# Performance work log

Hardware: AMD Instinct MI355X
Metric: run time of the kernel (lower is better)

The kernel has to match this reference:

```python
import jax, jax.numpy as jnp
import numpy as np

IN_CH, OUT_CH, KH, KW = 512, 512, 3, 3
LR_MULT = 1.0
WEIGHT_SCALE = LR_MULT / np.sqrt(IN_CH * KH * KW)


def setup_inputs() -> dict:
    key = jax.random.key(0)
    k1, k2, k3 = jax.random.split(key, 3)
    x = jax.random.normal(k1, (16, IN_CH, 32, 32), dtype=jnp.float32)
    s = jax.random.normal(k2, (16, IN_CH), dtype=jnp.float32)
    weight = jax.random.normal(k3, (OUT_CH, IN_CH, KH, KW), dtype=jnp.float32) / LR_MULT
    return {"x": x, "s": s, "weight": weight}


def reference(x, s, weight):
    B, Cin, H, Wd = x.shape
    Cout = weight.shape[0]
    W = weight * WEIGHT_SCALE                          # [Cout, Cin, kH, kW]
    # per-sample modulation: [B, Cout, Cin, kH, kW]
    Wm = s[:, None, :, None, None] * W[None]
    # demodulation: normalize each (b, out_channel) filter
    sigma = jnp.sqrt(jnp.sum(Wm ** 2, axis=(-3, -2, -1), keepdims=True) + 1e-8)
    Wm = Wm / sigma
    # grouped conv with groups = B
    x_g = x.reshape(1, B * Cin, H, Wd)
    W_g = Wm.reshape(B * Cout, Cin, KH, KW)
    out = jax.lax.conv_general_dilated(
        x_g, W_g,
        window_strides=(1, 1),
        padding="SAME",
        rhs_dilation=(1, 1),
        feature_group_count=B,
        dimension_numbers=("NCHW", "OIHW", "NCHW"),
    )
    return out.reshape(B, Cout, out.shape[-2], out.shape[-1])
```

## Files before the change

kernel.cpp:

```cpp
#include <hip/hip_runtime.h>
#include <hip/hip_bf16.h>


typedef __attribute__((ext_vector_type(4))) float f32x4;
typedef __attribute__((ext_vector_type(8))) short bf16x8;

#define NB    16
#define CIN   512
#define COUT  512
#define KTOT  4608
#define NPIX  (NB * 32 * 32)

__device__ __forceinline__ void gload_lds16(const void* g, void* l) {
  __builtin_amdgcn_global_load_lds(
      (__attribute__((address_space(1))) void*)(g),
      (__attribute__((address_space(3))) void*)(l), 16, 0, 0);
}

__global__ __launch_bounds__(256) void pack_w_kernel(
    const float* __restrict__ w, __hip_bfloat16* __restrict__ wB,
    float* __restrict__ wsq) {
  const int idx = blockIdx.x * 256 + threadIdx.x;
  const int o = idx >> 9, ci = idx & 511;
  const float* wp = w + (size_t)idx * 9;
  const float WSCALE = 0.014731391274719739f;
  float sum = 0.f;
#pragma unroll
  for (int t = 0; t < 9; ++t) {
    float v = wp[t] * WSCALE;
    sum += v * v;
    wB[(size_t)o * KTOT + t * 512 + ci] = __float2bfloat16(v);
  }
  wsq[idx] = sum;
}

__global__ __launch_bounds__(256) void calc_rsig_kernel(
    const float* __restrict__ s, const float* __restrict__ wsq,
    float* __restrict__ rsig) {
  const int wid = blockIdx.x * 4 + (threadIdx.x >> 6);
  const int lane = threadIdx.x & 63;
  const int b = wid >> 9, o = wid & 511;
  const float* sp = s + b * 512;
  const float* wp = wsq + o * 512;
  float sum = 0.f;
#pragma unroll
  for (int i = 0; i < 8; ++i) {
    float sv = sp[lane + i * 64];
    sum += sv * sv * wp[lane + i * 64];
  }
#pragma unroll
  for (int off = 32; off > 0; off >>= 1) sum += __shfl_down(sum, off, 64);
  if (lane == 0) rsig[wid] = 1.0f / sqrtf(sum + 1e-8f);
}

__global__ __launch_bounds__(256) void modulate_kernel(
    const float* __restrict__ x, const float* __restrict__ s,
    __hip_bfloat16* __restrict__ xpad) {
  const int by = blockIdx.x;
  const int b = by >> 5, y = by & 31;
  __shared__ __attribute__((aligned(16))) __hip_bfloat16 tile[32][72];
  const int tid = threadIdx.x;
  const int xc = tid & 31;
  const int cr0 = tid >> 5;
  const float* xrow = x + ((size_t)b * 512 * 32 + y) * 32;
  const float* sb = s + b * 512;
  __hip_bfloat16* orow = xpad + (size_t)((b * 34 + y + 1) * 34) * 512;

  for (int ci0 = 0; ci0 < 512; ci0 += 64) {
#pragma unroll
    for (int r = 0; r < 8; ++r) {
      const int cir = r * 8 + cr0;
      const int ci = ci0 + cir;
      float v = xrow[(size_t)ci * 1024 + xc] * sb[ci];
      tile[xc][cir] = __float2bfloat16(v);
    }
    __syncthreads();
    const int xcw = tid >> 3, vec = tid & 7;
    bf16x8 v = *(const bf16x8*)&tile[xcw][vec * 8];
    *(bf16x8*)(orow + (size_t)(xcw + 1) * 512 + ci0 + vec * 8) = v;
    __syncthreads();
  }
}

__global__ __launch_bounds__(256, 2) void conv_gemm_kernel(
    const __hip_bfloat16* __restrict__ wB,
    const __hip_bfloat16* __restrict__ xpad,
    const float* __restrict__ rsig,
    float* __restrict__ out,
    __hip_bfloat16* __restrict__ p1) {
  __shared__ __attribute__((aligned(16))) __hip_bfloat16 ldsA[128 * 64];
  __shared__ __attribute__((aligned(16))) __hip_bfloat16 ldsB[256 * 64];

  const int tid = threadIdx.x;
  const int wv = tid >> 6, lane = tid & 63, l15 = lane & 15;
  const int bo0 = blockIdx.y << 7;
  const int bp0 = blockIdx.x << 8;
  const int z = blockIdx.z;
  const int bimg = blockIdx.x >> 2;
  const int wr = wv >> 1, wc = wv & 1;

  int gA[4];
#pragma unroll
  for (int r = 0; r < 4; ++r) {
    const int c = r * 256 + tid, row = c >> 3, sc = (c & 7) ^ (row & 7);
    gA[r] = (bo0 + row) * KTOT + sc * 8;
  }
  int gB[8];
#pragma unroll
  for (int r = 0; r < 8; ++r) {
    const int c = r * 256 + tid, row = c >> 3, sc = (c & 7) ^ (row & 7);
    const int p = bp0 + row, b = p >> 10, rem = p & 1023, y = rem >> 5,
              xx = rem & 31;
    gB[r] = ((b * 34 + y) * 34 + xx) * 512 + sc * 8;
  }

  f32x4 acc[4][8];
#pragma unroll
  for (int mi = 0; mi < 4; ++mi)
#pragma unroll
    for (int ni = 0; ni < 8; ++ni) acc[mi][ni] = f32x4{0.f, 0.f, 0.f, 0.f};

  const int kb0 = (lane >> 4) << 4;

#pragma unroll 1
  for (int kt = 0; kt < 36; ++kt) {
    const int ktg = z * 36 + kt;
    const int tap = ktg >> 3;
    const int xoff = (tap + 31 * (tap / 3)) * 512 + ((ktg & 7) << 6);
#pragma unroll
    for (int r = 0; r < 4; ++r)
      gload_lds16(wB + (size_t)(gA[r] + (ktg << 6)),
                  (char*)ldsA + (r * 256 + tid) * 16);
#pragma unroll
    for (int r = 0; r < 8; ++r)
      gload_lds16(xpad + (size_t)(gB[r] + xoff),
                  (char*)ldsB + (r * 256 + tid) * 16);
    __syncthreads();

    bf16x8 af[4][2];
#pragma unroll
    for (int mi = 0; mi < 4; ++mi) {
      const int row = (wr << 6) + (mi << 4) + l15;
      const int swz = (row & 7) << 4;
      af[mi][0] = *(const bf16x8*)((const char*)ldsA + row * 128 + (kb0 ^ swz));
      af[mi][1] = *(const bf16x8*)((const char*)ldsA + row * 128 + ((64 | kb0) ^ swz));
    }
    {
      bf16x8 bv[8];
#pragma unroll
      for (int ni = 0; ni < 8; ++ni) {
        const int row = (wc << 7) + (ni << 4) + l15;
        bv[ni] = *(const bf16x8*)((const char*)ldsB + row * 128 +
                                  (kb0 ^ ((row & 7) << 4)));
      }
#pragma unroll
      for (int mi = 0; mi < 4; ++mi)
#pragma unroll
        for (int ni = 0; ni < 8; ++ni)
          acc[mi][ni] = __builtin_amdgcn_mfma_f32_16x16x32_bf16(
              af[mi][0], bv[ni], acc[mi][ni], 0, 0, 0);
    }
    {
      bf16x8 bv[8];
#pragma unroll
      for (int ni = 0; ni < 8; ++ni) {
        const int row = (wc << 7) + (ni << 4) + l15;
        bv[ni] = *(const bf16x8*)((const char*)ldsB + row * 128 +
                                  ((64 | kb0) ^ ((row & 7) << 4)));
      }
#pragma unroll
      for (int mi = 0; mi < 4; ++mi)
#pragma unroll
        for (int ni = 0; ni < 8; ++ni)
          acc[mi][ni] = __builtin_amdgcn_mfma_f32_16x16x32_bf16(
              af[mi][1], bv[ni], acc[mi][ni], 0, 0, 0);
    }
    __syncthreads();
  }

#pragma unroll
  for (int mi = 0; mi < 4; ++mi) {
    const int o = bo0 + (wr << 6) + (mi << 4) + ((lane >> 4) << 2);
    const f32x4 rs = *(const f32x4*)(rsig + (bimg << 9) + o);
#pragma unroll
    for (int ni = 0; ni < 8; ++ni) {
      const int p = bp0 + (wc << 7) + (ni << 4) + l15;
      const int prem = p & 1023;
      if (z == 0) {
#pragma unroll
        for (int r = 0; r < 4; ++r)
          out[((size_t)(bimg << 9) + o + r) * 1024 + prem] =
              acc[mi][ni][r] * rs[r];
      } else {
#pragma unroll
        for (int r = 0; r < 4; ++r)
          p1[((size_t)(bimg << 9) + o + r) * 1024 + prem] =
              __float2bfloat16(acc[mi][ni][r] * rs[r]);
      }
    }
  }
}

__global__ __launch_bounds__(256) void merge_kernel(
    float* __restrict__ out, const __hip_bfloat16* __restrict__ p1) {
  const int i = blockIdx.x * 256 + threadIdx.x;
  f32x4* o4 = (f32x4*)out + 2 * (size_t)i;
  f32x4 a = o4[0], b = o4[1];
  const bf16x8 pv = ((const bf16x8*)p1)[i];
#pragma unroll
  for (int j = 0; j < 4; ++j) {
    a[j] += __uint_as_float(((unsigned)(unsigned short)pv[j]) << 16);
    b[j] += __uint_as_float(((unsigned)(unsigned short)pv[4 + j]) << 16);
  }
  o4[0] = a;
  o4[1] = b;
}

extern "C" void kernel_launch(void* const* d_in, const int* in_sizes, int n_in,
                              void* d_out, int out_size, void* d_ws,
                              size_t ws_size, hipStream_t stream) {
  const float* x = (const float*)d_in[0];
  const float* s = (const float*)d_in[1];
  const float* w = (const float*)d_in[2];
  float* out = (float*)d_out;

  char* ws = (char*)d_ws;
  const size_t xpad_bytes = (size_t)NB * 34 * 34 * 512 * 2;
  const size_t wB_bytes = (size_t)COUT * KTOT * 2;
  const size_t wsq_bytes = (size_t)COUT * CIN * 4;
  const size_t rsig_bytes = (size_t)NB * COUT * 4;
  __hip_bfloat16* xpad = (__hip_bfloat16*)ws;
  __hip_bfloat16* wB = (__hip_bfloat16*)(ws + xpad_bytes);
  float* wsq = (float*)(ws + xpad_bytes + wB_bytes);
  float* rsig = (float*)(ws + xpad_bytes + wB_bytes + wsq_bytes);
  __hip_bfloat16* p1 =
      (__hip_bfloat16*)(ws + xpad_bytes + wB_bytes + wsq_bytes + rsig_bytes);

  hipMemsetAsync(xpad, 0, xpad_bytes, stream);
  pack_w_kernel<<<(COUT * CIN) / 256, 256, 0, stream>>>(w, wB, wsq);
  modulate_kernel<<<NB * 32, 256, 0, stream>>>(x, s, xpad);
  calc_rsig_kernel<<<(NB * COUT) / 4, 256, 0, stream>>>(s, wsq, rsig);
  conv_gemm_kernel<<<dim3(NPIX / 256, COUT / 128, 2), 256, 0, stream>>>(
      wB, xpad, rsig, out, p1);
  merge_kernel<<<(NPIX * COUT / 8) / 256, 256, 0, stream>>>(out, p1);
}
```

Baseline: 105.6 us.

## Drop split-K and merge kernel; add triple-buffered LDS prefetch pipeline

Measured after the change: 112.3 us. +6.3%, slower.

```diff
diff --git a/kernel.cpp b/kernel.cpp
--- a/kernel.cpp
+++ b/kernel.cpp
@@ -10,6 +10,13 @@
 #define COUT  512
 #define KTOT  4608
 #define NPIX  (NB * 32 * 32)
+#define KTILES 72
+#define BUFBYTES 49152
+
+#define WAITV12() asm volatile("s_waitcnt vmcnt(12)" ::: "memory")
+#define WAITV0()  asm volatile("s_waitcnt vmcnt(0)" ::: "memory")
+#define FENCE()   asm volatile("" ::: "memory")
+#define BAR()     { FENCE(); __builtin_amdgcn_s_barrier(); FENCE(); }
 
 __device__ __forceinline__ void gload_lds16(const void* g, void* l) {
   __builtin_amdgcn_global_load_lds(
@@ -82,20 +89,17 @@
   }
 }
 
-__global__ __launch_bounds__(256, 2) void conv_gemm_kernel(
+__global__ __launch_bounds__(256, 1) void conv_gemm_kernel(
     const __hip_bfloat16* __restrict__ wB,
     const __hip_bfloat16* __restrict__ xpad,
     const float* __restrict__ rsig,
-    float* __restrict__ out,
-    __hip_bfloat16* __restrict__ p1) {
-  __shared__ __attribute__((aligned(16))) __hip_bfloat16 ldsA[128 * 64];
-  __shared__ __attribute__((aligned(16))) __hip_bfloat16 ldsB[256 * 64];
+    float* __restrict__ out) {
+  extern __shared__ __attribute__((aligned(16))) char ldsc[];
 
   const int tid = threadIdx.x;
   const int wv = tid >> 6, lane = tid & 63, l15 = lane & 15;
   const int bo0 = blockIdx.y << 7;
   const int bp0 = blockIdx.x << 8;
-  const int z = blockIdx.z;
   const int bimg = blockIdx.x >> 2;
   const int wr = wv >> 1, wc = wv & 1;
 
@@ -114,44 +118,54 @@
     gB[r] = ((b * 34 + y) * 34 + xx) * 512 + sc * 8;
   }
 
-  f32x4 acc[4][8];
-#pragma unroll
-  for (int mi = 0; mi < 4; ++mi)
-#pragma unroll
-    for (int ni = 0; ni < 8; ++ni) acc[mi][ni] = f32x4{0.f, 0.f, 0.f, 0.f};
-
-  const int kb0 = (lane >> 4) << 4;
-
-#pragma unroll 1
-  for (int kt = 0; kt < 36; ++kt) {
-    const int ktg = z * 36 + kt;
-    const int tap = ktg >> 3;
-    const int xoff = (tap + 31 * (tap / 3)) * 512 + ((ktg & 7) << 6);
+  auto stage = [&](int kt) {
+    char* base = ldsc + (kt % 3) * BUFBYTES;
+    const int tap = kt >> 3;
+    const int xoff = (tap + 31 * (tap / 3)) * 512 + ((kt & 7) << 6);
 #pragma unroll
     for (int r = 0; r < 4; ++r)
-      gload_lds16(wB + (size_t)(gA[r] + (ktg << 6)),
-                  (char*)ldsA + (r * 256 + tid) * 16);
+      gload_lds16(wB + (size_t)(gA[r] + (kt << 6)),
+                  base + (r * 256 + tid) * 16);
 #pragma unroll
     for (int r = 0; r < 8; ++r)
       gload_lds16(xpad + (size_t)(gB[r] + xoff),
-                  (char*)ldsB + (r * 256 + tid) * 16);
-    __syncthreads();
+                  base + 16384 + (r * 256 + tid) * 16);
+  };
+
+  f32x4 acc[4][8];
+#pragma unroll
+  for (int mi = 0; mi < 4; ++mi)
+#pragma unroll
+    for (int ni = 0; ni < 8; ++ni) acc[mi][ni] = f32x4{0.f, 0.f, 0.f, 0.f};
+
+  const int kb0 = (lane >> 4) << 4;
+
+  stage(0);
+  stage(1);
+
+#pragma unroll 1
+  for (int kt = 0; kt < KTILES; ++kt) {
+    if (kt < KTILES - 1) { WAITV12(); } else { WAITV0(); }
+    BAR();
+    if (kt + 2 < KTILES) stage(kt + 2);
+
+    const char* bufA = ldsc + (kt % 3) * BUFBYTES;
+    const char* bufB = bufA + 16384;
 
     bf16x8 af[4][2];
 #pragma unroll
     for (int mi = 0; mi < 4; ++mi) {
       const int row = (wr << 6) + (mi << 4) + l15;
       const int swz = (row & 7) << 4;
-      af[mi][0] = *(const bf16x8*)((const char*)ldsA + row * 128 + (kb0 ^ swz));
-      af[mi][1] = *(const bf16x8*)((const char*)ldsA + row * 128 + ((64 | kb0) ^ swz));
+      af[mi][0] = *(const bf16x8*)(bufA + row * 128 + (kb0 ^ swz));
+      af[mi][1] = *(const bf16x8*)(bufA + row * 128 + ((64 | kb0) ^ swz));
     }
     {
       bf16x8 bv[8];
 #pragma unroll
       for (int ni = 0; ni < 8; ++ni) {
         const int row = (wc << 7) + (ni << 4) + l15;
-        bv[ni] = *(const bf16x8*)((const char*)ldsB + row * 128 +
-                                  (kb0 ^ ((row & 7) << 4)));
+        bv[ni] = *(const bf16x8*)(bufB + row * 128 + (kb0 ^ ((row & 7) << 4)));
       }
 #pragma unroll
       for (int mi = 0; mi < 4; ++mi)
@@ -165,7 +179,7 @@
 #pragma unroll
       for (int ni = 0; ni < 8; ++ni) {
         const int row = (wc << 7) + (ni << 4) + l15;
-        bv[ni] = *(const bf16x8*)((const char*)ldsB + row * 128 +
+        bv[ni] = *(const bf16x8*)(bufB + row * 128 +
                                   ((64 | kb0) ^ ((row & 7) << 4)));
       }
 #pragma unroll
@@ -175,7 +189,6 @@
           acc[mi][ni] = __builtin_amdgcn_mfma_f32_16x16x32_bf16(
               af[mi][1], bv[ni], acc[mi][ni], 0, 0, 0);
     }
-    __syncthreads();
   }
 
 #pragma unroll
@@ -186,34 +199,12 @@
     for (int ni = 0; ni < 8; ++ni) {
       const int p = bp0 + (wc << 7) + (ni << 4) + l15;
       const int prem = p & 1023;
-      if (z == 0) {
-#pragma unroll
-        for (int r = 0; r < 4; ++r)
-          out[((size_t)(bimg << 9) + o + r) * 1024 + prem] =
-              acc[mi][ni][r] * rs[r];
-      } else {
-#pragma unroll
-        for (int r = 0; r < 4; ++r)
-          p1[((size_t)(bimg << 9) + o + r) * 1024 + prem] =
-              __float2bfloat16(acc[mi][ni][r] * rs[r]);
-      }
-    }
-  }
-}
-
-__global__ __launch_bounds__(256) void merge_kernel(
-    float* __restrict__ out, const __hip_bfloat16* __restrict__ p1) {
-  const int i = blockIdx.x * 256 + threadIdx.x;
-  f32x4* o4 = (f32x4*)out + 2 * (size_t)i;
-  f32x4 a = o4[0], b = o4[1];
-  const bf16x8 pv = ((const bf16x8*)p1)[i];
-#pragma unroll
-  for (int j = 0; j < 4; ++j) {
-    a[j] += __uint_as_float(((unsigned)(unsigned short)pv[j]) << 16);
-    b[j] += __uint_as_float(((unsigned)(unsigned short)pv[4 + j]) << 16);
-  }
-  o4[0] = a;
-  o4[1] = b;
+#pragma unroll
+      for (int r = 0; r < 4; ++r)
+        out[((size_t)(bimg << 9) + o + r) * 1024 + prem] =
+            acc[mi][ni][r] * rs[r];
+    }
+  }
 }
 
 extern "C" void kernel_launch(void* const* d_in, const int* in_sizes, int n_in,
@@ -228,19 +219,19 @@
   const size_t xpad_bytes = (size_t)NB * 34 * 34 * 512 * 2;
   const size_t wB_bytes = (size_t)COUT * KTOT * 2;
   const size_t wsq_bytes = (size_t)COUT * CIN * 4;
-  const size_t rsig_bytes = (size_t)NB * COUT * 4;
   __hip_bfloat16* xpad = (__hip_bfloat16*)ws;
   __hip_bfloat16* wB = (__hip_bfloat16*)(ws + xpad_bytes);
   float* wsq = (float*)(ws + xpad_bytes + wB_bytes);
   float* rsig = (float*)(ws + xpad_bytes + wB_bytes + wsq_bytes);
-  __hip_bfloat16* p1 =
-      (__hip_bfloat16*)(ws + xpad_bytes + wB_bytes + wsq_bytes + rsig_bytes);
+
+  const int lds_bytes = 3 * BUFBYTES;
+  hipFuncSetAttribute((const void*)conv_gemm_kernel,
+                      hipFuncAttributeMaxDynamicSharedMemorySize, lds_bytes);
 
   hipMemsetAsync(xpad, 0, xpad_bytes, stream);
   pack_w_kernel<<<(COUT * CIN) / 256, 256, 0, stream>>>(w, wB, wsq);
   modulate_kernel<<<NB * 32, 256, 0, stream>>>(x, s, xpad);
   calc_rsig_kernel<<<(NB * COUT) / 4, 256, 0, stream>>>(s, wsq, rsig);
-  conv_gemm_kernel<<<dim3(NPIX / 256, COUT / 128, 2), 256, 0, stream>>>(
-      wB, xpad, rsig, out, p1);
-  merge_kernel<<<(NPIX * COUT / 8) / 256, 256, 0, stream>>>(out, p1);
-}
+  conv_gemm_kernel<<<dim3(NPIX / 256, COUT / 128), 256, lds_bytes, stream>>>(
+      wB, xpad, rsig, out);
+}
```

## Switch conv GEMM to 32x32x16 MFMA with fragment-ordered LDS, halo-only zeroing, bf16 partials

Applied to the files above, without the earlier changes.

Result: slower. 142.3 us (+34.8%).

```diff
diff --git a/kernel.cpp b/kernel.cpp
--- a/kernel.cpp
+++ b/kernel.cpp
@@ -3,6 +3,7 @@
 
 
 typedef __attribute__((ext_vector_type(4))) float f32x4;
+typedef __attribute__((ext_vector_type(16))) float f32x16;
 typedef __attribute__((ext_vector_type(8))) short bf16x8;
 
 #define NB    16
@@ -15,6 +16,10 @@
   __builtin_amdgcn_global_load_lds(
       (__attribute__((address_space(1))) void*)(g),
       (__attribute__((address_space(3))) void*)(l), 16, 0, 0);
+}
+
+__device__ __forceinline__ float bf16bits_to_f32(short v) {
+  return __uint_as_float(((unsigned)(unsigned short)v) << 16);
 }
 
 __global__ __launch_bounds__(256) void pack_w_kernel(
@@ -82,17 +87,31 @@
   }
 }
 
+__global__ __launch_bounds__(256) void halo_zero_kernel(
+    __hip_bfloat16* __restrict__ xpad) {
+  const int sb = blockIdx.x;
+  const int b = sb / 132, s = sb - b * 132;
+  int y, x;
+  if (s < 34)       { y = 0;        x = s; }
+  else if (s < 68)  { y = 33;       x = s - 34; }
+  else if (s < 100) { y = s - 67;   x = 0; }
+  else              { y = s - 99;   x = 33; }
+  unsigned* p = (unsigned*)(xpad + (size_t)((b * 34 + y) * 34 + x) * 512);
+  p[threadIdx.x] = 0u;
+}
+
 __global__ __launch_bounds__(256, 2) void conv_gemm_kernel(
     const __hip_bfloat16* __restrict__ wB,
     const __hip_bfloat16* __restrict__ xpad,
     const float* __restrict__ rsig,
     float* __restrict__ out,
+    __hip_bfloat16* __restrict__ p0,
     __hip_bfloat16* __restrict__ p1) {
-  __shared__ __attribute__((aligned(16))) __hip_bfloat16 ldsA[128 * 64];
-  __shared__ __attribute__((aligned(16))) __hip_bfloat16 ldsB[256 * 64];
+  __shared__ __attribute__((aligned(16))) char ldsc[49152];
 
   const int tid = threadIdx.x;
-  const int wv = tid >> 6, lane = tid & 63, l15 = lane & 15;
+  const int wv = tid >> 6, lane = tid & 63;
+  const int l31 = lane & 31, lhi = lane >> 5;
   const int bo0 = blockIdx.y << 7;
   const int bp0 = blockIdx.x << 8;
   const int z = blockIdx.z;
@@ -102,25 +121,29 @@
   int gA[4];
 #pragma unroll
   for (int r = 0; r < 4; ++r) {
-    const int c = r * 256 + tid, row = c >> 3, sc = (c & 7) ^ (row & 7);
-    gA[r] = (bo0 + row) * KTOT + sc * 8;
+    const int u = r * 256 + tid, frag = u >> 6, l = u & 63;
+    const int fi = frag >> 2, ks = frag & 3;
+    const int row = fi * 32 + (l & 31), k = ks * 16 + (l >> 5) * 8;
+    gA[r] = (bo0 + row) * KTOT + k;
   }
   int gB[8];
 #pragma unroll
   for (int r = 0; r < 8; ++r) {
-    const int c = r * 256 + tid, row = c >> 3, sc = (c & 7) ^ (row & 7);
-    const int p = bp0 + row, b = p >> 10, rem = p & 1023, y = rem >> 5,
+    const int u = r * 256 + tid, frag = u >> 6, l = u & 63;
+    const int ni = frag >> 2, ks = frag & 3;
+    const int pr = ni * 32 + (l & 31), k = ks * 16 + (l >> 5) * 8;
+    const int p = bp0 + pr, b = p >> 10, rem = p & 1023, y = rem >> 5,
               xx = rem & 31;
-    gB[r] = ((b * 34 + y) * 34 + xx) * 512 + sc * 8;
-  }
-
-  f32x4 acc[4][8];
-#pragma unroll
-  for (int mi = 0; mi < 4; ++mi)
-#pragma unroll
-    for (int ni = 0; ni < 8; ++ni) acc[mi][ni] = f32x4{0.f, 0.f, 0.f, 0.f};
-
-  const int kb0 = (lane >> 4) << 4;
+    gB[r] = ((b * 34 + y) * 34 + xx) * 512 + k;
+  }
+
+  f32x16 acc[2][4];
+#pragma unroll
+  for (int mi = 0; mi < 2; ++mi)
+#pragma unroll
+    for (int ni = 0; ni < 4; ++ni)
+#pragma unroll
+      for (int e = 0; e < 16; ++e) acc[mi][ni][e] = 0.f;
 
 #pragma unroll 1
   for (int kt = 0; kt < 36; ++kt) {
@@ -130,87 +153,89 @@
 #pragma unroll
     for (int r = 0; r < 4; ++r)
       gload_lds16(wB + (size_t)(gA[r] + (ktg << 6)),
-                  (char*)ldsA + (r * 256 + tid) * 16);
+                  ldsc + (r * 256 + tid) * 16);
 #pragma unroll
     for (int r = 0; r < 8; ++r)
       gload_lds16(xpad + (size_t)(gB[r] + xoff),
-                  (char*)ldsB + (r * 256 + tid) * 16);
-    __syncthreads();
-
-    bf16x8 af[4][2];
-#pragma unroll
-    for (int mi = 0; mi < 4; ++mi) {
-      const int row = (wr << 6) + (mi << 4) + l15;
-      const int swz = (row & 7) << 4;
-      af[mi][0] = *(const bf16x8*)((const char*)ldsA + row * 128 + (kb0 ^ swz));
-      af[mi][1] = *(const bf16x8*)((const char*)ldsA + row * 128 + ((64 | kb0) ^ swz));
+                  ldsc + 16384 + (r * 256 + tid) * 16);
+    __syncthreads();
+
+    bf16x8 av[2][4];
+#pragma unroll
+    for (int mi = 0; mi < 2; ++mi)
+#pragma unroll
+      for (int ks = 0; ks < 4; ++ks)
+        av[mi][ks] = *(const bf16x8*)(
+            ldsc + (((wr * 2 + mi) * 4 + ks) << 10) + lane * 16);
+#pragma unroll
+    for (int ks = 0; ks < 4; ++ks) {
+      bf16x8 bv[4];
+#pragma unroll
+      for (int ni = 0; ni < 4; ++ni)
+        bv[ni] = *(const bf16x8*)(
+            ldsc + 16384 + (((wc * 4 + ni) * 4 + ks) << 10) + lane * 16);
+#pragma unroll
+      for (int mi = 0; mi < 2; ++mi)
+#pragma unroll
+        for (int ni = 0; ni < 4; ++ni)
+          acc[mi][ni] = __builtin_amdgcn_mfma_f32_32x32x16_bf16(
+              av[mi][ks], bv[ni], acc[mi][ni], 0, 0, 0);
     }
-    {
-      bf16x8 bv[8];
-#pragma unroll
-      for (int ni = 0; ni < 8; ++ni) {
-        const int row = (wc << 7) + (ni << 4) + l15;
-        bv[ni] = *(const bf16x8*)((const char*)ldsB + row * 128 +
-                                  (kb0 ^ ((row & 7) << 4)));
-      }
-#pragma unroll
-      for (int mi = 0; mi < 4; ++mi)
-#pragma unroll
-        for (int ni = 0; ni < 8; ++ni)
-          acc[mi][ni] = __builtin_amdgcn_mfma_f32_16x16x32_bf16(
-              af[mi][0], bv[ni], acc[mi][ni], 0, 0, 0);
-    }
-    {
-      bf16x8 bv[8];
-#pragma unroll
-      for (int ni = 0; ni < 8; ++ni) {
-        const int row = (wc << 7) + (ni << 4) + l15;
-        bv[ni] = *(const bf16x8*)((const char*)ldsB + row * 128 +
-                                  ((64 | kb0) ^ ((row & 7) << 4)));
-      }
-#pragma unroll
-      for (int mi = 0; mi < 4; ++mi)
-#pragma unroll
-        for (int ni = 0; ni < 8; ++ni)
-          acc[mi][ni] = __builtin_amdgcn_mfma_f32_16x16x32_bf16(
-              af[mi][1], bv[ni], acc[mi][ni], 0, 0, 0);
-    }
-    __syncthreads();
-  }
-
-#pragma unroll
-  for (int mi = 0; mi < 4; ++mi) {
-    const int o = bo0 + (wr << 6) + (mi << 4) + ((lane >> 4) << 2);
-    const f32x4 rs = *(const f32x4*)(rsig + (bimg << 9) + o);
-#pragma unroll
-    for (int ni = 0; ni < 8; ++ni) {
-      const int p = bp0 + (wc << 7) + (ni << 4) + l15;
-      const int prem = p & 1023;
-      if (z == 0) {
-#pragma unroll
-        for (int r = 0; r < 4; ++r)
-          out[((size_t)(bimg << 9) + o + r) * 1024 + prem] =
-              acc[mi][ni][r] * rs[r];
-      } else {
-#pragma unroll
-        for (int r = 0; r < 4; ++r)
-          p1[((size_t)(bimg << 9) + o + r) * 1024 + prem] =
-              __float2bfloat16(acc[mi][ni][r] * rs[r]);
+    __syncthreads();
+  }
+
+  __hip_bfloat16* pz = z ? p1 : p0;
+  const bool f32path = (p0 == nullptr) && (z == 0);
+#pragma unroll
+  for (int mi = 0; mi < 2; ++mi) {
+    const int obase = bo0 + (wr << 6) + (mi << 5);
+#pragma unroll
+    for (int q = 0; q < 4; ++q) {
+      const int r4 = q * 8 + lhi * 4;
+      const f32x4 rs = *(const f32x4*)(rsig + (bimg << 9) + obase + r4);
+#pragma unroll
+      for (int ni = 0; ni < 4; ++ni) {
+        const int p = bp0 + (wc << 7) + (ni << 5) + l31;
+        const int prem = p & 1023;
+#pragma unroll
+        for (int j = 0; j < 4; ++j) {
+          const float v = acc[mi][ni][q * 4 + j] * rs[j];
+          const size_t oidx =
+              ((size_t)((bimg << 9) + obase + r4 + j)) * 1024 + prem;
+          if (f32path) out[oidx] = v;
+          else pz[oidx] = __float2bfloat16(v);
+        }
       }
     }
   }
 }
 
-__global__ __launch_bounds__(256) void merge_kernel(
+__global__ __launch_bounds__(256) void merge2_kernel(
+    float* __restrict__ out, const __hip_bfloat16* __restrict__ p0,
+    const __hip_bfloat16* __restrict__ p1) {
+  const size_t i = (size_t)blockIdx.x * 256 + threadIdx.x;
+  const bf16x8 a = ((const bf16x8*)p0)[i];
+  const bf16x8 b = ((const bf16x8*)p1)[i];
+  f32x4 o0, o1;
+#pragma unroll
+  for (int j = 0; j < 4; ++j) {
+    o0[j] = bf16bits_to_f32(a[j]) + bf16bits_to_f32(b[j]);
+    o1[j] = bf16bits_to_f32(a[4 + j]) + bf16bits_to_f32(b[4 + j]);
+  }
+  ((f32x4*)out)[2 * i] = o0;
+  ((f32x4*)out)[2 * i + 1] = o1;
+}
+
+__global__ __launch_bounds__(256) void merge1_kernel(
     float* __restrict__ out, const __hip_bfloat16* __restrict__ p1) {
-  const int i = blockIdx.x * 256 + threadIdx.x;
-  f32x4* o4 = (f32x4*)out + 2 * (size_t)i;
+  const size_t i = (size_t)blockIdx.x * 256 + threadIdx.x;
+  f32x4* o4 = (f32x4*)out + 2 * i;
   f32x4 a = o4[0], b = o4[1];
   const bf16x8 pv = ((const bf16x8*)p1)[i];
 #pragma unroll
   for (int j = 0; j < 4; ++j) {
-    a[j] += __uint_as_float(((unsigned)(unsigned short)pv[j]) << 16);
-    b[j] += __uint_as_float(((unsigned)(unsigned short)pv[4 + j]) << 16);
+    a[j] += bf16bits_to_f32(pv[j]);
+    b[j] += bf16bits_to_f32(pv[4 + j]);
   }
   o4[0] = a;
   o4[1] = b;
@@ -229,18 +254,27 @@
   const size_t wB_bytes = (size_t)COUT * KTOT * 2;
   const size_t wsq_bytes = (size_t)COUT * CIN * 4;
   const size_t rsig_bytes = (size_t)NB * COUT * 4;
+  const size_t part_bytes = (size_t)NPIX * COUT * 2;
   __hip_bfloat16* xpad = (__hip_bfloat16*)ws;
   __hip_bfloat16* wB = (__hip_bfloat16*)(ws + xpad_bytes);
   float* wsq = (float*)(ws + xpad_bytes + wB_bytes);
   float* rsig = (float*)(ws + xpad_bytes + wB_bytes + wsq_bytes);
-  __hip_bfloat16* p1 =
-      (__hip_bfloat16*)(ws + xpad_bytes + wB_bytes + wsq_bytes + rsig_bytes);
-
-  hipMemsetAsync(xpad, 0, xpad_bytes, stream);
+  char* pbase = ws + xpad_bytes + wB_bytes + wsq_bytes + rsig_bytes;
+  __hip_bfloat16* p1 = (__hip_bfloat16*)pbase;
+  __hip_bfloat16* p0 = (__hip_bfloat16*)(pbase + part_bytes);
+  const bool two_partials =
+      ws_size >= (xpad_bytes + wB_bytes + wsq_bytes + rsig_bytes +
+                  2 * part_bytes);
+
+  halo_zero_kernel<<<NB * 132, 256, 0, stream>>>(xpad);
   pack_w_kernel<<<(COUT * CIN) / 256, 256, 0, stream>>>(w, wB, wsq);
   modulate_kernel<<<NB * 32, 256, 0, stream>>>(x, s, xpad);
   calc_rsig_kernel<<<(NB * COUT) / 4, 256, 0, stream>>>(s, wsq, rsig);
   conv_gemm_kernel<<<dim3(NPIX / 256, COUT / 128, 2), 256, 0, stream>>>(
-      wB, xpad, rsig, out, p1);
-  merge_kernel<<<(NPIX * COUT / 8) / 256, 256, 0, stream>>>(out, p1);
-}
+      wB, xpad, rsig, out, two_partials ? p0 : nullptr, p1);
+  const int mblocks = (NPIX * COUT / 8) / 256;
+  if (two_partials)
+    merge2_kernel<<<mblocks, 256, 0, stream>>>(out, p0, p1);
+  else
+    merge1_kernel<<<mblocks, 256, 0, stream>>>(out, p1);
+}
```

## Split conv GEMM K into three slices, zero only halo, raise occupancy hint

Applied to the files above, without the earlier changes.

New measurement: 149.3 us. +41.3%, slower.

```diff
diff --git a/kernel.cpp b/kernel.cpp
--- a/kernel.cpp
+++ b/kernel.cpp
@@ -15,6 +15,10 @@
   __builtin_amdgcn_global_load_lds(
       (__attribute__((address_space(1))) void*)(g),
       (__attribute__((address_space(3))) void*)(l), 16, 0, 0);
+}
+
+__device__ __forceinline__ float bf16bits_to_f32(short v) {
+  return __uint_as_float(((unsigned)(unsigned short)v) << 16);
 }
 
 __global__ __launch_bounds__(256) void pack_w_kernel(
@@ -82,12 +86,28 @@
   }
 }
 
-__global__ __launch_bounds__(256, 2) void conv_gemm_kernel(
+__global__ __launch_bounds__(256) void halo_zero_kernel(
+    __hip_bfloat16* __restrict__ xpad) {
+  const int sb = blockIdx.x;
+  const int b = sb / 132, s = sb - b * 132;
+  int y, x;
+  if (s < 34)       { y = 0;        x = s; }
+  else if (s < 68)  { y = 33;       x = s - 34; }
+  else if (s < 100) { y = s - 67;   x = 0; }
+  else              { y = s - 99;   x = 33; }
+  unsigned* p = (unsigned*)(xpad + (size_t)((b * 34 + y) * 34 + x) * 512);
+  p[threadIdx.x] = 0u;
+}
+
+__global__ __launch_bounds__(256, 3) void conv_gemm_kernel(
     const __hip_bfloat16* __restrict__ wB,
     const __hip_bfloat16* __restrict__ xpad,
     const float* __restrict__ rsig,
     float* __restrict__ out,
-    __hip_bfloat16* __restrict__ p1) {
+    __hip_bfloat16* __restrict__ p0,
+    __hip_bfloat16* __restrict__ p1,
+    __hip_bfloat16* __restrict__ p2,
+    int ktpz) {
   __shared__ __attribute__((aligned(16))) __hip_bfloat16 ldsA[128 * 64];
   __shared__ __attribute__((aligned(16))) __hip_bfloat16 ldsB[256 * 64];
 
@@ -96,6 +116,7 @@
   const int bo0 = blockIdx.y << 7;
   const int bp0 = blockIdx.x << 8;
   const int z = blockIdx.z;
+  const int zbase = z * ktpz;
   const int bimg = blockIdx.x >> 2;
   const int wr = wv >> 1, wc = wv & 1;
 
@@ -123,8 +144,8 @@
   const int kb0 = (lane >> 4) << 4;
 
 #pragma unroll 1
-  for (int kt = 0; kt < 36; ++kt) {
-    const int ktg = z * 36 + kt;
+  for (int kt = 0; kt < ktpz; ++kt) {
+    const int ktg = zbase + kt;
     const int tap = ktg >> 3;
     const int xoff = (tap + 31 * (tap / 3)) * 512 + ((ktg & 7) << 6);
 #pragma unroll
@@ -178,6 +199,8 @@
     __syncthreads();
   }
 
+  __hip_bfloat16* pz = (z == 0) ? p0 : ((z == 1) ? p1 : p2);
+  const bool f32path = (p0 == nullptr) && (z == 0);
 #pragma unroll
   for (int mi = 0; mi < 4; ++mi) {
     const int o = bo0 + (wr << 6) + (mi << 4) + ((lane >> 4) << 2);
@@ -186,31 +209,63 @@
     for (int ni = 0; ni < 8; ++ni) {
       const int p = bp0 + (wc << 7) + (ni << 4) + l15;
       const int prem = p & 1023;
-      if (z == 0) {
-#pragma unroll
-        for (int r = 0; r < 4; ++r)
-          out[((size_t)(bimg << 9) + o + r) * 1024 + prem] =
-              acc[mi][ni][r] * rs[r];
-      } else {
-#pragma unroll
-        for (int r = 0; r < 4; ++r)
-          p1[((size_t)(bimg << 9) + o + r) * 1024 + prem] =
-              __float2bfloat16(acc[mi][ni][r] * rs[r]);
+#pragma unroll
+      for (int r = 0; r < 4; ++r) {
+        const float v = acc[mi][ni][r] * rs[r];
+        const size_t oidx = ((size_t)((bimg << 9) + o + r)) * 1024 + prem;
+        if (f32path) out[oidx] = v;
+        else pz[oidx] = __float2bfloat16(v);
       }
     }
   }
 }
 
-__global__ __launch_bounds__(256) void merge_kernel(
+__global__ __launch_bounds__(256) void merge3_kernel(
+    float* __restrict__ out, const __hip_bfloat16* __restrict__ p0,
+    const __hip_bfloat16* __restrict__ p1,
+    const __hip_bfloat16* __restrict__ p2) {
+  const size_t i = (size_t)blockIdx.x * 256 + threadIdx.x;
+  const bf16x8 a = ((const bf16x8*)p0)[i];
+  const bf16x8 b = ((const bf16x8*)p1)[i];
+  const bf16x8 c = ((const bf16x8*)p2)[i];
+  f32x4 o0, o1;
+#pragma unroll
+  for (int j = 0; j < 4; ++j) {
+    o0[j] = bf16bits_to_f32(a[j]) + bf16bits_to_f32(b[j]) +
+            bf16bits_to_f32(c[j]);
+    o1[j] = bf16bits_to_f32(a[4 + j]) + bf16bits_to_f32(b[4 + j]) +
+            bf16bits_to_f32(c[4 + j]);
+  }
+  ((f32x4*)out)[2 * i] = o0;
+  ((f32x4*)out)[2 * i + 1] = o1;
+}
+
+__global__ __launch_bounds__(256) void merge2_kernel(
+    float* __restrict__ out, const __hip_bfloat16* __restrict__ p0,
+    const __hip_bfloat16* __restrict__ p1) {
+  const size_t i = (size_t)blockIdx.x * 256 + threadIdx.x;
+  const bf16x8 a = ((const bf16x8*)p0)[i];
+  const bf16x8 b = ((const bf16x8*)p1)[i];
+  f32x4 o0, o1;
+#pragma unroll
+  for (int j = 0; j < 4; ++j) {
+    o0[j] = bf16bits_to_f32(a[j]) + bf16bits_to_f32(b[j]);
+    o1[j] = bf16bits_to_f32(a[4 + j]) + bf16bits_to_f32(b[4 + j]);
+  }
+  ((f32x4*)out)[2 * i] = o0;
+  ((f32x4*)out)[2 * i + 1] = o1;
+}
+
+__global__ __launch_bounds__(256) void merge1_kernel(
     float* __restrict__ out, const __hip_bfloat16* __restrict__ p1) {
-  const int i = blockIdx.x * 256 + threadIdx.x;
-  f32x4* o4 = (f32x4*)out + 2 * (size_t)i;
+  const size_t i = (size_t)blockIdx.x * 256 + threadIdx.x;
+  f32x4* o4 = (f32x4*)out + 2 * i;
   f32x4 a = o4[0], b = o4[1];
   const bf16x8 pv = ((const bf16x8*)p1)[i];
 #pragma unroll
   for (int j = 0; j < 4; ++j) {
-    a[j] += __uint_as_float(((unsigned)(unsigned short)pv[j]) << 16);
-    b[j] += __uint_as_float(((unsigned)(unsigned short)pv[4 + j]) << 16);
+    a[j] += bf16bits_to_f32(pv[j]);
+    b[j] += bf16bits_to_f32(pv[4 + j]);
   }
   o4[0] = a;
   o4[1] = b;
@@ -229,18 +284,35 @@
   const size_t wB_bytes = (size_t)COUT * KTOT * 2;
   const size_t wsq_bytes = (size_t)COUT * CIN * 4;
   const size_t rsig_bytes = (size_t)NB * COUT * 4;
+  const size_t part_bytes = (size_t)NPIX * COUT * 2;
+  const size_t base_bytes = xpad_bytes + wB_bytes + wsq_bytes + rsig_bytes;
   __hip_bfloat16* xpad = (__hip_bfloat16*)ws;
   __hip_bfloat16* wB = (__hip_bfloat16*)(ws + xpad_bytes);
   float* wsq = (float*)(ws + xpad_bytes + wB_bytes);
   float* rsig = (float*)(ws + xpad_bytes + wB_bytes + wsq_bytes);
-  __hip_bfloat16* p1 =
-      (__hip_bfloat16*)(ws + xpad_bytes + wB_bytes + wsq_bytes + rsig_bytes);
-
-  hipMemsetAsync(xpad, 0, xpad_bytes, stream);
+  __hip_bfloat16* pa = (__hip_bfloat16*)(ws + base_bytes);
+  __hip_bfloat16* pb = (__hip_bfloat16*)(ws + base_bytes + part_bytes);
+  __hip_bfloat16* pc = (__hip_bfloat16*)(ws + base_bytes + 2 * part_bytes);
+  const bool fits3 = ws_size >= base_bytes + 3 * part_bytes;
+  const bool fits2 = ws_size >= base_bytes + 2 * part_bytes;
+
+  halo_zero_kernel<<<NB * 132, 256, 0, stream>>>(xpad);
   pack_w_kernel<<<(COUT * CIN) / 256, 256, 0, stream>>>(w, wB, wsq);
   modulate_kernel<<<NB * 32, 256, 0, stream>>>(x, s, xpad);
   calc_rsig_kernel<<<(NB * COUT) / 4, 256, 0, stream>>>(s, wsq, rsig);
-  conv_gemm_kernel<<<dim3(NPIX / 256, COUT / 128, 2), 256, 0, stream>>>(
-      wB, xpad, rsig, out, p1);
-  merge_kernel<<<(NPIX * COUT / 8) / 256, 256, 0, stream>>>(out, p1);
-}
+
+  const int mblocks = (NPIX * COUT / 8) / 256;
+  if (fits3) {
+    conv_gemm_kernel<<<dim3(NPIX / 256, COUT / 128, 3), 256, 0, stream>>>(
+        wB, xpad, rsig, out, pa, pb, pc, 24);
+    merge3_kernel<<<mblocks, 256, 0, stream>>>(out, pa, pb, pc);
+  } else if (fits2) {
+    conv_gemm_kernel<<<dim3(NPIX / 256, COUT / 128, 2), 256, 0, stream>>>(
+        wB, xpad, rsig, out, pa, pb, nullptr, 36);
+    merge2_kernel<<<mblocks, 256, 0, stream>>>(out, pa, pb);
+  } else {
+    conv_gemm_kernel<<<dim3(NPIX / 256, COUT / 128, 2), 256, 0, stream>>>(
+        wB, xpad, rsig, out, nullptr, pa, nullptr, 36);
+    merge1_kernel<<<mblocks, 256, 0, stream>>>(out, pa);
+  }
+}
```
